# Kernel optimization log

Hardware: AMD Instinct MI355X
Metric: run time of the kernel (lower is better)

Reference implementation:

```python
import jax, jax.numpy as jnp
import numpy as np

G, M, K = 4096, 50, 30          # graphs, nodes per graph, sort-pool k
H, NUM_LAYERS, F_IN = 32, 3, 128
DEG = 8
N = G * M
E = N * DEG
D_LAT = H * NUM_LAYERS + 1       # 97 = conv1d kernel/stride
DENSE_DIM = (((K - 2) // 2 + 1) - 5 + 1) * 32  # 352


def setup_inputs() -> dict:
    key = jax.random.key(0)
    ks = jax.random.split(key, 14)
    x = jax.random.normal(ks[0], (N, F_IN), dtype=jnp.float32)
    # graph-local random edges so each subgraph is self-contained
    offs = (jnp.arange(E, dtype=jnp.int32) // (M * DEG)) * M
    src = jax.random.randint(ks[1], (E,), 0, M, dtype=jnp.int32) + offs
    dst = jax.random.randint(ks[2], (E,), 0, M, dtype=jnp.int32) + offs
    edge_index = jnp.stack([src, dst])
    batch = jnp.repeat(jnp.arange(G, dtype=jnp.int32), M)

    def lin(k, i, o):
        return (jax.random.normal(k, (i, o), dtype=jnp.float32) / np.sqrt(i)).astype(jnp.float32)

    W0, b0 = lin(ks[3], F_IN, H), jnp.zeros((H,), jnp.float32)
    W1, b1 = lin(ks[4], H, H), jnp.zeros((H,), jnp.float32)
    W2, b2 = lin(ks[5], H, H), jnp.zeros((H,), jnp.float32)
    W3, b3 = lin(ks[6], H, 1), jnp.zeros((1,), jnp.float32)
    C1w = (jax.random.normal(ks[7], (16, 1, D_LAT)) / np.sqrt(D_LAT)).astype(jnp.float32)
    C1b = jnp.zeros((16,), jnp.float32)
    C2w = (jax.random.normal(ks[8], (32, 16, 5)) / np.sqrt(16 * 5)).astype(jnp.float32)
    C2b = jnp.zeros((32,), jnp.float32)
    L1w, L1b = lin(ks[9], DENSE_DIM, 128), jnp.zeros((128,), jnp.float32)
    L2w, L2b = lin(ks[10], 128, 1), jnp.zeros((1,), jnp.float32)
    return {"x": x, "edge_index": edge_index, "batch": batch,
            "W0": W0, "b0": b0, "W1": W1, "b1": b1, "W2": W2, "b2": b2,
            "W3": W3, "b3": b3, "C1w": C1w, "C1b": C1b, "C2w": C2w, "C2b": C2b,
            "L1w": L1w, "L1b": L1b, "L2w": L2w, "L2b": L2b}


def _gcn_norm(edge_index, n):
    # add self loops, symmetric normalization (PyG GCNConv default)
    loop = jnp.arange(n, dtype=edge_index.dtype)
    src = jnp.concatenate([edge_index[0], loop])
    dst = jnp.concatenate([edge_index[1], loop])
    deg = jax.ops.segment_sum(jnp.ones_like(dst, dtype=jnp.float32), dst, num_segments=n)
    dinv = jnp.where(deg > 0, deg ** -0.5, 0.0)
    return src, dst, dinv[src] * dinv[dst]


def _gcn_conv(h, W, b, src, dst, norm, n):
    h = h @ W                                    # [N, out]
    msg = h[src] * norm[:, None]                 # gather + weight
    return jax.ops.segment_sum(msg, dst, num_segments=n) + b


def reference(x, edge_index, batch, W0, b0, W1, b1, W2, b2, W3, b3,
              C1w, C1b, C2w, C2b, L1w, L1b, L2w, L2b):
    n = x.shape[0]
    src, dst, norm = _gcn_norm(edge_index, n)
    h1 = jnp.tanh(_gcn_conv(x, W0, b0, src, dst, norm, n))
    h2 = jnp.tanh(_gcn_conv(h1, W1, b1, src, dst, norm, n))
    h3 = jnp.tanh(_gcn_conv(h2, W2, b2, src, dst, norm, n))
    h4 = jnp.tanh(_gcn_conv(h3, W3, b3, src, dst, norm, n))
    lat = jnp.concatenate([h1, h2, h3, h4], axis=-1)      # [N, 97]
    # global_sort_pool: graphs are contiguous equal-size blocks (batch = arange(G).repeat(M)),
    # sort nodes within each graph by last channel, descending, keep top K
    xd = lat.reshape(G, M, D_LAT)
    order = jnp.argsort(-xd[..., -1], axis=1)             # [G, M]
    xs = jnp.take_along_axis(xd, order[..., None], axis=1)[:, :K]  # [G, K, 97]
    # Conv1d(1,16,97,stride=97) on [G,1,K*97] == per-slot linear over the 97 latent dims
    z = jnp.einsum('gtd,cd->gct', xs, C1w[:, 0, :]) + C1b[None, :, None]  # [G,16,K]
    z = jax.nn.relu(z)
    z = z.reshape(G, 16, K // 2, 2).max(axis=-1)          # MaxPool1d(2,2) -> [G,16,15]
    z = jax.lax.conv_general_dilated(z, C2w, window_strides=(1,), padding='VALID',
                                     dimension_numbers=('NCH', 'OIH', 'NCH'))
    z = jax.nn.relu(z + C2b[None, :, None])               # [G,32,11]
    z = z.reshape(G, -1)                                  # [G,352]
    z = jax.nn.relu(z @ L1w + L1b)
    # dropout: eval mode (identity)
    return z @ L2w + L2b                                  # [G,1]
```

## Files before the change

kernel.cpp:

```cpp
#include <hip/hip_runtime.h>
#include <math.h>

#define NG 4096
#define M 50
#define KTOP 30
#define H 32
#define F_IN 128
#define EPG 400
#define E_TOTAL (NG * EPG)
#define DLAT 97
#define LATS 100
#define NTHREADS 256

template <int KIN>
__device__ __forceinline__ void gcn_matmul(const float* hin, int istride,
                                           const float* __restrict__ W,
                                           float (*tb)[H], int tid) {
    const int j = tid & 31, iset = tid >> 5;
    float acc[7];
    int rows[7];
#pragma unroll
    for (int r = 0; r < 7; r++) {
        acc[r] = 0.f;
        int i = iset + r * 8;
        rows[r] = (i >= M) ? (M - 1) : i;
    }
#pragma unroll 2
    for (int k4 = 0; k4 < KIN / 4; k4++) {
        const float w0 = W[(4 * k4 + 0) * H + j];
        const float w1 = W[(4 * k4 + 1) * H + j];
        const float w2 = W[(4 * k4 + 2) * H + j];
        const float w3 = W[(4 * k4 + 3) * H + j];
#pragma unroll
        for (int r = 0; r < 7; r++) {
            const float4 xv = *(const float4*)(hin + rows[r] * istride + 4 * k4);
            acc[r] += xv.x * w0 + xv.y * w1 + xv.z * w2 + xv.w * w3;
        }
    }
#pragma unroll
    for (int r = 0; r < 7; r++) {
        int i = iset + r * 8;
        if (i < M) tb[i][j] = acc[r];
    }
}

__device__ __forceinline__ void gcn_agg(const float (*tbuf)[H], const float* __restrict__ b,
                                        float (*lat)[LATS], int col0,
                                        const float* dinv, const int* csr_off,
                                        const int* csr_src, const float* csr_nrm, int tid) {
    const int j = tid & 31, iset = tid >> 5;
    for (int i = iset; i < M; i += 8) {
        float acc = tbuf[i][j] * dinv[i] * dinv[i];
        int e0 = csr_off[i], e1 = csr_off[i + 1];
        for (int e = e0; e < e1; e++)
            acc += tbuf[csr_src[e]][j] * csr_nrm[e];
        lat[i][col0 + j] = tanhf(acc + b[j]);
    }
}

__global__ __launch_bounds__(NTHREADS, 4)
void dgcnn_kernel(const float* __restrict__ x, const int* __restrict__ eidx,
                  const float* __restrict__ W0, const float* __restrict__ b0,
                  const float* __restrict__ W1, const float* __restrict__ b1,
                  const float* __restrict__ W2, const float* __restrict__ b2,
                  const float* __restrict__ W3, const float* __restrict__ b3,
                  const float* __restrict__ C1w, const float* __restrict__ C1b,
                  const float* __restrict__ C2w, const float* __restrict__ C2b,
                  const float* __restrict__ L1w, const float* __restrict__ L1b,
                  const float* __restrict__ L2w, const float* __restrict__ L2b,
                  float* __restrict__ out) {
    __shared__ __align__(16) float lat[M][LATS];
    __shared__ float tbuf[M][H];
    __shared__ union U {
        struct { int ls[EPG]; int ld[EPG]; } setup;
        struct {
            float z1[16][KTOP];
            float pbuf[16][15];
            float z2[352];
            float d1[128];
            float red[256];
            int   ord[M];
        } post;
    } u;
    __shared__ int   csr_off[M + 1], cursor[M];
    __shared__ int   csr_src[EPG];
    __shared__ float csr_nrm[EPG];
    __shared__ int   degi[M];
    __shared__ float dinv[M];

    const int g = blockIdx.x;
    const int tid = threadIdx.x;
    const int nbase = g * M;
    const int ebase = g * EPG;
    const float* xg = x + (size_t)nbase * F_IN;

    if (tid < M) degi[tid] = 1;
    __syncthreads();
    for (int e = tid; e < EPG; e += NTHREADS) {
        int s = eidx[ebase + e] - nbase;
        int d = eidx[E_TOTAL + ebase + e] - nbase;
        u.setup.ls[e] = s; u.setup.ld[e] = d;
        atomicAdd(&degi[d], 1);
    }
    __syncthreads();
    if (tid < M) dinv[tid] = rsqrtf((float)degi[tid]);
    if (tid < 64) {
        int cnt = (tid < M) ? (degi[tid] - 1) : 0;
        int incl = cnt;
#pragma unroll
        for (int off = 1; off < 64; off <<= 1) {
            int nv = __shfl_up(incl, off);
            if (tid >= off) incl += nv;
        }
        if (tid < M) { csr_off[tid] = incl - cnt; cursor[tid] = incl - cnt; }
        if (tid == M - 1) csr_off[M] = incl;
    }
    __syncthreads();
    for (int e = tid; e < EPG; e += NTHREADS) {
        int s = u.setup.ls[e], d = u.setup.ld[e];
        float nr = dinv[s] * dinv[d];
        int pos = atomicAdd(&cursor[d], 1);
        csr_src[pos] = s;
        csr_nrm[pos] = nr;
    }
    __syncthreads();

    gcn_matmul<F_IN>(xg, F_IN, W0, tbuf, tid);
    __syncthreads();
    gcn_agg(tbuf, b0, lat, 0, dinv, csr_off, csr_src, csr_nrm, tid);
    __syncthreads();
    gcn_matmul<H>(&lat[0][0], LATS, W1, tbuf, tid);
    __syncthreads();
    gcn_agg(tbuf, b1, lat, 32, dinv, csr_off, csr_src, csr_nrm, tid);
    __syncthreads();
    gcn_matmul<H>(&lat[0][32], LATS, W2, tbuf, tid);
    __syncthreads();
    gcn_agg(tbuf, b2, lat, 64, dinv, csr_off, csr_src, csr_nrm, tid);
    __syncthreads();
    if (tid < M) {
        float acc = 0.f;
        for (int k = 0; k < H; k++) acc += lat[tid][64 + k] * W3[k];
        tbuf[tid][0] = acc;
    }
    __syncthreads();
    if (tid < M) {
        float acc = tbuf[tid][0] * dinv[tid] * dinv[tid];
        int e0 = csr_off[tid], e1 = csr_off[tid + 1];
        for (int e = e0; e < e1; e++)
            acc += tbuf[csr_src[e]][0] * csr_nrm[e];
        lat[tid][96] = tanhf(acc + b3[0]);
    }
    __syncthreads();

    if (tid < M) {
        float v = lat[tid][96];
        int r = 0;
        for (int jj = 0; jj < M; jj++) {
            float vj = lat[jj][96];
            r += (vj > v) || (vj == v && jj < tid);
        }
        u.post.ord[r] = tid;
    }
    __syncthreads();

    for (int idx = tid; idx < 16 * KTOP; idx += NTHREADS) {
        int c = idx / KTOP, t = idx - c * KTOP;
        const float* row = lat[u.post.ord[t]];
        float acc = 0.f;
        for (int d = 0; d < DLAT; d++) acc += row[d] * C1w[c * DLAT + d];
        acc += C1b[c];
        u.post.z1[c][t] = fmaxf(acc, 0.f);
    }
    __syncthreads();

    for (int idx = tid; idx < 16 * 15; idx += NTHREADS) {
        int c = idx / 15, t = idx - c * 15;
        u.post.pbuf[c][t] = fmaxf(u.post.z1[c][2 * t], u.post.z1[c][2 * t + 1]);
    }
    __syncthreads();

    for (int idx = tid; idx < 352; idx += NTHREADS) {
        int o = idx / 11, t = idx - o * 11;
        float acc = C2b[o];
        for (int i = 0; i < 16; i++) {
#pragma unroll
            for (int k = 0; k < 5; k++)
                acc += u.post.pbuf[i][t + k] * C2w[(o * 16 + i) * 5 + k];
        }
        u.post.z2[idx] = fmaxf(acc, 0.f);
    }
    __syncthreads();

    {
        int jj = tid & 127, half = tid >> 7;
        float acc = (half == 0) ? L1b[jj] : 0.f;
        int f0 = half * 176;
        for (int f = f0; f < f0 + 176; f++)
            acc += u.post.z2[f] * L1w[f * 128 + jj];
        u.post.red[tid] = acc;
    }
    __syncthreads();
    if (tid < 128)
        u.post.d1[tid] = fmaxf(u.post.red[tid] + u.post.red[tid + 128], 0.f);
    __syncthreads();

    if (tid < 128) u.post.red[tid] = u.post.d1[tid] * L2w[tid];
    __syncthreads();
    if (tid < 64) {
        float v = u.post.red[tid] + u.post.red[tid + 64];
#pragma unroll
        for (int off = 32; off >= 1; off >>= 1)
            v += __shfl_down(v, off);
        if (tid == 0) out[g] = v + L2b[0];
    }
}

extern "C" void kernel_launch(void* const* d_in, const int* in_sizes, int n_in,
                              void* d_out, int out_size, void* d_ws, size_t ws_size,
                              hipStream_t stream) {
    const float* x    = (const float*)d_in[0];
    const int*   eidx = (const int*)d_in[1];
    dgcnn_kernel<<<NG, NTHREADS, 0, stream>>>(
        x, eidx,
        (const float*)d_in[3],  (const float*)d_in[4],
        (const float*)d_in[5],  (const float*)d_in[6],
        (const float*)d_in[7],  (const float*)d_in[8],
        (const float*)d_in[9],  (const float*)d_in[10],
        (const float*)d_in[11], (const float*)d_in[12],
        (const float*)d_in[13], (const float*)d_in[14],
        (const float*)d_in[15], (const float*)d_in[16],
        (const float*)d_in[17], (const float*)d_in[18],
        (float*)d_out);
}
```

Before: 428.2 us.

## Shrink shared memory, overlap first matmul with CSR setup, use fast tanh

Several changes at once. Shared memory is cut by storing CSR sources as bytes, dropping the staged edge arrays, reusing the degree array as the cursor and reorganising the post-processing union, and launch bounds are raised from 4 to 5 blocks per SM. The first matmul now runs inside the degree-counting phase, saving one barrier. Rows are given to threads in contiguous chunks of 7 or 6 instead of a strided clamped mapping, and tanhf is replaced by an exp-based approximation. The conv1 thread mapping is also changed and the final reductions are merged, at the cost of reading the edge list twice from global memory and slightly different tanh rounding.

```diff
diff --git a/kernel.cpp b/kernel.cpp
--- a/kernel.cpp
+++ b/kernel.cpp
@@ -12,19 +12,22 @@
 #define LATS 100
 #define NTHREADS 256
 
+__device__ __forceinline__ float fast_tanh(float x) {
+    x = fminf(fmaxf(x, -15.f), 15.f);
+    float e = __expf(2.f * x);
+    return 1.f - 2.f / (e + 1.f);
+}
+
 template <int KIN>
 __device__ __forceinline__ void gcn_matmul(const float* hin, int istride,
                                            const float* __restrict__ W,
                                            float (*tb)[H], int tid) {
     const int j = tid & 31, iset = tid >> 5;
+    const bool seven = (iset < 2);
+    const int base = seven ? 7 * iset : 14 + 6 * (iset - 2);
     float acc[7];
-    int rows[7];
-#pragma unroll
-    for (int r = 0; r < 7; r++) {
-        acc[r] = 0.f;
-        int i = iset + r * 8;
-        rows[r] = (i >= M) ? (M - 1) : i;
-    }
+#pragma unroll
+    for (int r = 0; r < 7; r++) acc[r] = 0.f;
 #pragma unroll 2
     for (int k4 = 0; k4 < KIN / 4; k4++) {
         const float w0 = W[(4 * k4 + 0) * H + j];
@@ -32,33 +35,36 @@
         const float w2 = W[(4 * k4 + 2) * H + j];
         const float w3 = W[(4 * k4 + 3) * H + j];
 #pragma unroll
-        for (int r = 0; r < 7; r++) {
-            const float4 xv = *(const float4*)(hin + rows[r] * istride + 4 * k4);
+        for (int r = 0; r < 6; r++) {
+            const float4 xv = *(const float4*)(hin + (base + r) * istride + 4 * k4);
             acc[r] += xv.x * w0 + xv.y * w1 + xv.z * w2 + xv.w * w3;
         }
-    }
-#pragma unroll
-    for (int r = 0; r < 7; r++) {
-        int i = iset + r * 8;
-        if (i < M) tb[i][j] = acc[r];
-    }
+        if (seven) {
+            const float4 xv = *(const float4*)(hin + (base + 6) * istride + 4 * k4);
+            acc[6] += xv.x * w0 + xv.y * w1 + xv.z * w2 + xv.w * w3;
+        }
+    }
+#pragma unroll
+    for (int r = 0; r < 6; r++) tb[base + r][j] = acc[r];
+    if (seven) tb[base + 6][j] = acc[6];
 }
 
 __device__ __forceinline__ void gcn_agg(const float (*tbuf)[H], const float* __restrict__ b,
                                         float (*lat)[LATS], int col0,
                                         const float* dinv, const int* csr_off,
-                                        const int* csr_src, const float* csr_nrm, int tid) {
+                                        const unsigned char* csr_src, const float* csr_nrm,
+                                        int tid) {
     const int j = tid & 31, iset = tid >> 5;
     for (int i = iset; i < M; i += 8) {
         float acc = tbuf[i][j] * dinv[i] * dinv[i];
         int e0 = csr_off[i], e1 = csr_off[i + 1];
         for (int e = e0; e < e1; e++)
             acc += tbuf[csr_src[e]][j] * csr_nrm[e];
-        lat[i][col0 + j] = tanhf(acc + b[j]);
-    }
-}
-
-__global__ __launch_bounds__(NTHREADS, 4)
+        lat[i][col0 + j] = fast_tanh(acc + b[j]);
+    }
+}
+
+__global__ __launch_bounds__(NTHREADS, 5)
 void dgcnn_kernel(const float* __restrict__ x, const int* __restrict__ eidx,
                   const float* __restrict__ W0, const float* __restrict__ b0,
                   const float* __restrict__ W1, const float* __restrict__ b1,
@@ -71,22 +77,18 @@
                   float* __restrict__ out) {
     __shared__ __align__(16) float lat[M][LATS];
     __shared__ float tbuf[M][H];
-    __shared__ union U {
-        struct { int ls[EPG]; int ld[EPG]; } setup;
-        struct {
-            float z1[16][KTOP];
-            float pbuf[16][15];
-            float z2[352];
-            float d1[128];
-            float red[256];
-            int   ord[M];
-        } post;
-    } u;
-    __shared__ int   csr_off[M + 1], cursor[M];
-    __shared__ int   csr_src[EPG];
     __shared__ float csr_nrm[EPG];
+    __shared__ unsigned char csr_src[EPG];
+    __shared__ int   csr_off[M + 1];
     __shared__ int   degi[M];
     __shared__ float dinv[M];
+    __shared__ struct Post {
+        float pbuf[16][15];
+        union {
+            struct { float z1[16][KTOP]; int ord[M]; } a;
+            struct { float z2[352]; float red[256]; } b;
+        } u;
+    } post;
 
     const int g = blockIdx.x;
     const int tid = threadIdx.x;
@@ -97,11 +99,10 @@
     if (tid < M) degi[tid] = 1;
     __syncthreads();
     for (int e = tid; e < EPG; e += NTHREADS) {
-        int s = eidx[ebase + e] - nbase;
         int d = eidx[E_TOTAL + ebase + e] - nbase;
-        u.setup.ls[e] = s; u.setup.ld[e] = d;
         atomicAdd(&degi[d], 1);
     }
+    gcn_matmul<F_IN>(xg, F_IN, W0, tbuf, tid);
     __syncthreads();
     if (tid < M) dinv[tid] = rsqrtf((float)degi[tid]);
     if (tid < 64) {
@@ -112,21 +113,20 @@
             int nv = __shfl_up(incl, off);
             if (tid >= off) incl += nv;
         }
-        if (tid < M) { csr_off[tid] = incl - cnt; cursor[tid] = incl - cnt; }
+        if (tid < M) { csr_off[tid] = incl - cnt; degi[tid] = incl - cnt; }
         if (tid == M - 1) csr_off[M] = incl;
     }
     __syncthreads();
     for (int e = tid; e < EPG; e += NTHREADS) {
-        int s = u.setup.ls[e], d = u.setup.ld[e];
+        int s = eidx[ebase + e] - nbase;
+        int d = eidx[E_TOTAL + ebase + e] - nbase;
         float nr = dinv[s] * dinv[d];
-        int pos = atomicAdd(&cursor[d], 1);
-        csr_src[pos] = s;
+        int pos = atomicAdd(&degi[d], 1);
+        csr_src[pos] = (unsigned char)s;
         csr_nrm[pos] = nr;
     }
     __syncthreads();
 
-    gcn_matmul<F_IN>(xg, F_IN, W0, tbuf, tid);
-    __syncthreads();
     gcn_agg(tbuf, b0, lat, 0, dinv, csr_off, csr_src, csr_nrm, tid);
     __syncthreads();
     gcn_matmul<H>(&lat[0][0], LATS, W1, tbuf, tid);
@@ -159,23 +159,23 @@
             float vj = lat[jj][96];
             r += (vj > v) || (vj == v && jj < tid);
         }
-        u.post.ord[r] = tid;
+        post.u.a.ord[r] = tid;
     }
     __syncthreads();
 
     for (int idx = tid; idx < 16 * KTOP; idx += NTHREADS) {
-        int c = idx / KTOP, t = idx - c * KTOP;
-        const float* row = lat[u.post.ord[t]];
+        int t = idx >> 4, c = idx & 15;
+        const float* row = lat[post.u.a.ord[t]];
         float acc = 0.f;
         for (int d = 0; d < DLAT; d++) acc += row[d] * C1w[c * DLAT + d];
         acc += C1b[c];
-        u.post.z1[c][t] = fmaxf(acc, 0.f);
+        post.u.a.z1[c][t] = fmaxf(acc, 0.f);
     }
     __syncthreads();
 
     for (int idx = tid; idx < 16 * 15; idx += NTHREADS) {
         int c = idx / 15, t = idx - c * 15;
-        u.post.pbuf[c][t] = fmaxf(u.post.z1[c][2 * t], u.post.z1[c][2 * t + 1]);
+        post.pbuf[c][t] = fmaxf(post.u.a.z1[c][2 * t], post.u.a.z1[c][2 * t + 1]);
     }
     __syncthreads();
 
@@ -185,9 +185,9 @@
         for (int i = 0; i < 16; i++) {
 #pragma unroll
             for (int k = 0; k < 5; k++)
-                acc += u.post.pbuf[i][t + k] * C2w[(o * 16 + i) * 5 + k];
-        }
-        u.post.z2[idx] = fmaxf(acc, 0.f);
+                acc += post.pbuf[i][t + k] * C2w[(o * 16 + i) * 5 + k];
+        }
+        post.u.b.z2[idx] = fmaxf(acc, 0.f);
     }
     __syncthreads();
 
@@ -196,18 +196,16 @@
         float acc = (half == 0) ? L1b[jj] : 0.f;
         int f0 = half * 176;
         for (int f = f0; f < f0 + 176; f++)
-            acc += u.post.z2[f] * L1w[f * 128 + jj];
-        u.post.red[tid] = acc;
+            acc += post.u.b.z2[f] * L1w[f * 128 + jj];
+        post.u.b.red[tid] = acc;
     }
     __syncthreads();
     if (tid < 128)
-        u.post.d1[tid] = fmaxf(u.post.red[tid] + u.post.red[tid + 128], 0.f);
-    __syncthreads();
-
-    if (tid < 128) u.post.red[tid] = u.post.d1[tid] * L2w[tid];
+        post.u.b.red[tid] = fmaxf(post.u.b.red[tid] + post.u.b.red[tid + 128], 0.f)
+                            * L2w[tid];
     __syncthreads();
     if (tid < 64) {
-        float v = u.post.red[tid] + u.post.red[tid + 64];
+        float v = post.u.b.red[tid] + post.u.b.red[tid + 64];
 #pragma unroll
         for (int off = 32; off >= 1; off >>= 1)
             v += __shfl_down(v, off);
```

Measured after the change: 507.3 us. 1.18x slower.
